# Performance work log

Hardware: AMD Instinct MI355X
Metric: run time of the kernel (lower is better)

Reference implementation:

```python
import jax, jax.numpy as jnp
import numpy as np

VOCAB = 32000
DIM = 1024
HID = 4096
MAXLEN = 2048
NH = 2       # number of sequential LowRankLinearAttention layers
KD = 64      # key_dim hardcoded in the module
B = 2
L = 2048


def setup_inputs() -> dict:
    key = jax.random.key(0)
    ks = jax.random.split(key, 12)
    def rn(k, shape, scale):
        return jax.random.normal(k, shape, dtype=jnp.float32) * scale
    return {
        "input_indices": jax.random.randint(ks[0], (B, L), 0, VOCAB),
        "token_embed": rn(ks[1], (VOCAB, DIM), 0.02),
        "pos_embed": rn(ks[2], (MAXLEN, DIM), 0.02),
        # per-layer attention projections (stored [in, out]; x @ W == torch Linear)
        "Wq": rn(ks[3], (NH, DIM, KD), DIM ** -0.5),
        "Wk": rn(ks[4], (NH, DIM, KD), DIM ** -0.5),
        "Wv": rn(ks[5], (NH, DIM, KD), DIM ** -0.5),
        "Wo": rn(ks[6], (NH, KD, DIM), KD ** -0.5),
        "norm_g": jnp.ones((NH, DIM), jnp.float32),
        "norm_b": jnp.zeros((NH, DIM), jnp.float32),
        "out_norm_g": jnp.ones((DIM,), jnp.float32),
        "out_norm_b": jnp.zeros((DIM,), jnp.float32),
        "W1": rn(ks[7], (DIM, HID), DIM ** -0.5),
        "b1": jnp.zeros((HID,), jnp.float32),
        "W2": rn(ks[8], (HID, VOCAB), HID ** -0.5),
        "b2": jnp.zeros((VOCAB,), jnp.float32),
    }


def _layernorm(x, g, b, eps=1e-5):
    m = jnp.mean(x, axis=-1, keepdims=True)
    v = jnp.var(x, axis=-1, keepdims=True)
    return (x - m) / jnp.sqrt(v + eps) * g + b


def _lowrank_linear_attn(x, Wq, Wk, Wv, Wo):
    # x: [B,L,D]; Q,K,V: [B,L,k]
    Q = jax.nn.elu(x @ Wq) + 1.0
    K = jax.nn.elu(x @ Wk) + 1.0
    V = x @ Wv
    # causal prefix sums of outer products K_t V_t^T -> [B,L,k,k]
    KV_sum = jnp.cumsum(K[..., :, None] * V[..., None, :], axis=1)
    K_sum = jnp.cumsum(K, axis=1)
    num = jnp.einsum('blk,blkj->blj', Q, KV_sum)          # [B,L,k]
    den = jnp.einsum('blk,blk->bl', Q, K_sum)[..., None]  # [B,L,1]
    return (num / (den + 1e-6)) @ Wo


def reference(input_indices, token_embed, pos_embed, Wq, Wk, Wv, Wo,
              norm_g, norm_b, out_norm_g, out_norm_b, W1, b1, W2, b2):
    seq_len = input_indices.shape[1]
    x = token_embed[input_indices] + pos_embed[jnp.arange(seq_len)]
    for i in range(Wq.shape[0]):
        x = x + _lowrank_linear_attn(x, Wq[i], Wk[i], Wv[i], Wo[i])
        x = _layernorm(x, norm_g[i], norm_b[i])
    x = _layernorm(x, out_norm_g, out_norm_b)
    h = jax.nn.gelu(x @ W1 + b1, approximate=False)  # torch nn.GELU default = erf
    logits = h @ W2 + b2
    return logits
```

## Files before the change

### kernel.cpp

```cpp
#include <hip/hip_runtime.h>

typedef __attribute__((ext_vector_type(4))) float  f4;
typedef __attribute__((ext_vector_type(2))) float  f2;
typedef __attribute__((ext_vector_type(4))) unsigned short us4;
typedef __attribute__((ext_vector_type(8))) short  s8;
typedef __attribute__((ext_vector_type(4))) float  f32x4;

__device__ __forceinline__ unsigned short f2bf(float f) {
  unsigned u = __float_as_uint(f);
  u += 0x7fffu + ((u >> 16) & 1u);
  return (unsigned short)(u >> 16);
}
__device__ __forceinline__ float elu1(float x) { return x > 0.f ? x + 1.f : __expf(x); }
__device__ __forceinline__ float gelu_erf(float x) { return 0.5f * x * (1.f + erff(x * 0.70710678118654752f)); }

__device__ __forceinline__ void async16(const void* g, void* l) {
  __builtin_amdgcn_global_load_lds((const __attribute__((address_space(1))) void*)g,
                                   (__attribute__((address_space(3))) void*)l, 16, 0, 0);
}

__device__ __forceinline__ unsigned l2u(const void* p) {
  return (unsigned)(size_t)(const __attribute__((address_space(3))) char*)p;
}
template<int OFF>
__device__ __forceinline__ void dsr(s8& d, unsigned base) {
  asm volatile("ds_read_b128 %0, %1 offset:%2" : "=v"(d) : "v"(base), "i"(OFF));
}
template<int KB>
__device__ __forceinline__ void readA8(s8 (&af)[8], unsigned base) {
  dsr<(0 * 2 + KB) * 1024>(af[0], base);
  dsr<(1 * 2 + KB) * 1024>(af[1], base);
  dsr<(2 * 2 + KB) * 1024>(af[2], base);
  dsr<(3 * 2 + KB) * 1024>(af[3], base);
  dsr<(4 * 2 + KB) * 1024>(af[4], base);
  dsr<(5 * 2 + KB) * 1024>(af[5], base);
  dsr<(6 * 2 + KB) * 1024>(af[6], base);
  dsr<(7 * 2 + KB) * 1024>(af[7], base);
}

__global__ __launch_bounds__(256) void embed_kernel(
    const int* __restrict__ idx, const float* __restrict__ tok,
    const float* __restrict__ pos, float* __restrict__ X, unsigned short* __restrict__ XB)
{
  int g = blockIdx.x * 256 + threadIdx.x;
  int t = g >> 8;
  int c4 = (g & 255) * 4;
  int l = t & 2047;
  int tk = idx[t];
  f4 v = *(const f4*)(tok + (size_t)tk * 1024 + c4);
  f4 p = *(const f4*)(pos + (size_t)l * 1024 + c4);
  v += p;
  *(f4*)(X + (size_t)t * 1024 + c4) = v;
  us4 o = { f2bf(v[0]), f2bf(v[1]), f2bf(v[2]), f2bf(v[3]) };
  *(us4*)(XB + (size_t)t * 1024 + c4) = o;
}

__global__ __launch_bounds__(256) void transpose_cvt(
    const float* __restrict__ src, unsigned short* __restrict__ dst, int N, int K)
{
  __shared__ unsigned short t[64][72];
  int k0 = blockIdx.x * 64, n0 = blockIdx.y * 64;
  int tid = threadIdx.x;
#pragma unroll
  for (int i = 0; i < 4; ++i) {
    int f = tid + i * 256;
    int r = f >> 4, c4 = (f & 15) * 4;
    f4 v = *(const f4*)(src + (size_t)(k0 + r) * N + n0 + c4);
    us4 o = { f2bf(v[0]), f2bf(v[1]), f2bf(v[2]), f2bf(v[3]) };
    *(us4*)&t[r][c4] = o;
  }
  __syncthreads();
#pragma unroll
  for (int i = 0; i < 4; ++i) {
    int f = tid + i * 256;
    int nr = f >> 4, kc4 = (f & 15) * 4;
    us4 o = { t[kc4 + 0][nr], t[kc4 + 1][nr], t[kc4 + 2][nr], t[kc4 + 3][nr] };
    *(us4*)(dst + (size_t)(n0 + nr) * K + k0 + kc4) = o;
  }
}

template<int EPI, int BF32>
__global__ __launch_bounds__(256) void gemm_bt(
    const unsigned short* __restrict__ A, const unsigned short* __restrict__ Bt,
    const float* __restrict__ Bf, const float* __restrict__ bias,
    void* __restrict__ Cv, int M, int N, int K, int mtiles)
{
  __shared__ unsigned short As[128 * 32];
  __shared__ unsigned short Bs[128 * 32];
  int bid = blockIdx.x;
  int mt = bid % mtiles, nt = bid / mtiles;
  int m0 = mt * 128, n0 = nt * 128;
  int tid = threadIdx.x, lane = tid & 63, w = tid >> 6;
  int wm = (w & 1) * 64, wn = (w >> 1) * 64;

  int c0 = w * 128 + lane, c1 = c0 + 64;
  size_t aO0 = (size_t)(m0 + (c0 >> 2)) * K + (size_t)((c0 & 3) * 8);
  size_t aO1 = (size_t)(m0 + (c1 >> 2)) * K + (size_t)((c1 & 3) * 8);
  size_t bO0 = (size_t)(n0 + (c0 >> 2)) * K + (size_t)((c0 & 3) * 8);
  size_t bO1 = (size_t)(n0 + (c1 >> 2)) * K + (size_t)((c1 & 3) * 8);
  unsigned short* lA0 = As + (w * 128) * 8;
  unsigned short* lA1 = As + (w * 128 + 64) * 8;
  unsigned short* lB0 = Bs + (w * 128) * 8;
  unsigned short* lB1 = Bs + (w * 128 + 64) * 8;

  f32x4 acc[4][4];
  f32x4 zz = {0.f, 0.f, 0.f, 0.f};
#pragma unroll
  for (int i = 0; i < 4; ++i)
#pragma unroll
    for (int j = 0; j < 4; ++j) acc[i][j] = zz;

  int rr = lane & 15, kh = (lane >> 4) * 8;
  const unsigned short* Ar = As + (wm + rr) * 32 + kh;
  const unsigned short* Br = Bs + (wn + rr) * 32 + kh;

  for (int k0 = 0; k0 < K; k0 += 32) {
    async16(A + aO0 + k0, lA0);
    async16(A + aO1 + k0, lA1);
    if constexpr (!BF32) {
      async16(Bt + bO0 + k0, lB0);
      async16(Bt + bO1 + k0, lB1);
    } else {
#pragma unroll
      for (int i = 0; i < 4; ++i) {
        int f = tid + i * 256;
        int kr = f >> 5, c4 = (f & 31) * 4;
        f4 v = *(const f4*)(Bf + (size_t)(k0 + kr) * N + n0 + c4);
#pragma unroll
        for (int e = 0; e < 4; ++e) Bs[(c4 + e) * 32 + kr] = f2bf(v[e]);
      }
    }
    __syncthreads();
    s8 af[4], bfr[4];
#pragma unroll
    for (int mi = 0; mi < 4; ++mi) af[mi] = *(const s8*)(Ar + mi * 512);
#pragma unroll
    for (int ni = 0; ni < 4; ++ni) bfr[ni] = *(const s8*)(Br + ni * 512);
#pragma unroll
    for (int mi = 0; mi < 4; ++mi)
#pragma unroll
      for (int ni = 0; ni < 4; ++ni)
        acc[mi][ni] = __builtin_amdgcn_mfma_f32_16x16x32_bf16(af[mi], bfr[ni], acc[mi][ni], 0, 0, 0);
    __syncthreads();
  }

  int cr = (lane >> 4) * 4;
#pragma unroll
  for (int mi = 0; mi < 4; ++mi) {
#pragma unroll
    for (int ni = 0; ni < 4; ++ni) {
      int gc = n0 + wn + ni * 16 + rr;
      float bv = (EPI > 0) ? bias[gc] : 0.f;
#pragma unroll
      for (int r = 0; r < 4; ++r) {
        int gr = m0 + wm + mi * 16 + cr + r;
        float v = acc[mi][ni][r] + bv;
        if constexpr (EPI == 1) {
          ((unsigned short*)Cv)[(size_t)gr * N + gc] = f2bf(gelu_erf(v));
        } else {
          ((float*)Cv)[(size_t)gr * N + gc] = v;
        }
      }
    }
  }
}

template<int RA, int RDKB, int RDNH, int ACCN, typename STG>
__device__ __forceinline__ void phaseX(
    unsigned ArdB, unsigned BrdB,
    s8 (&afDst)[8], s8 (&bfDst)[2],
    const s8 (&afUse)[8], const s8 (&bfUse)[2],
    f32x4 (&acc)[8][4], STG stg)
{
  dsr<((RDNH * 2 + 0) * 2 + RDKB) * 1024>(bfDst[0], BrdB);
  dsr<((RDNH * 2 + 1) * 2 + RDKB) * 1024>(bfDst[1], BrdB);
  if constexpr (RA) readA8<RDKB>(afDst, ArdB);
  stg();
  asm volatile("s_waitcnt vmcnt(6)" ::: "memory");
  __builtin_amdgcn_s_barrier();
  if constexpr (RA) asm volatile("s_waitcnt lgkmcnt(10)" ::: "memory");
  else              asm volatile("s_waitcnt lgkmcnt(2)" ::: "memory");
  __builtin_amdgcn_sched_barrier(0);
  __builtin_amdgcn_s_setprio(1);
#pragma unroll
  for (int f = 0; f < 8; ++f) {
    acc[f][ACCN * 2 + 0] =
        __builtin_amdgcn_mfma_f32_16x16x32_bf16(afUse[f], bfUse[0], acc[f][ACCN * 2 + 0], 0, 0, 0);
    acc[f][ACCN * 2 + 1] =
        __builtin_amdgcn_mfma_f32_16x16x32_bf16(afUse[f], bfUse[1], acc[f][ACCN * 2 + 1], 0, 0, 0);
  }
  __builtin_amdgcn_s_setprio(0);
  __builtin_amdgcn_sched_barrier(0);
}

template<int EPI>
__global__ __launch_bounds__(512, 2) void gemm256(
    const unsigned short* __restrict__ A, const unsigned short* __restrict__ Bt,
    const float* __restrict__ bias, void* __restrict__ Cv,
    int M, int N, int K, int mtiles)
{
  __shared__ __align__(16) char A0r[32768];
  __shared__ __align__(16) char B0r[32768];
  __shared__ __align__(16) char A1r[32768];
  __shared__ __align__(16) char B1r[32768];

  const int tid = threadIdx.x, lane = tid & 63, w = tid >> 6;
  const int wm = w >> 2, wn = w & 3;
  const int NT = K >> 6;

  int nwg = gridDim.x, orig = blockIdx.x;
  int q = nwg >> 3, r = nwg & 7;
  int xcd = orig & 7, lin = orig >> 3;
  int swz = (xcd < r ? xcd * (q + 1) : r * (q + 1) + (xcd - r) * q) + lin;
  int mt = swz % mtiles, nt = swz / mtiles;
  int m0 = mt * 256, n0 = nt * 256;

  const size_t klane8 = (size_t)((lane >> 4) << 3);
  const size_t arow0 = (size_t)(m0 + w * 32 + (lane & 15)) * K;
  const size_t arow1 = arow0 + (size_t)16 * K;
  const size_t brow0 = (size_t)(n0 + w * 32 + (lane & 15)) * K;
  const size_t brow1 = brow0 + (size_t)16 * K;
  const int stgoff = w * 4096;

  auto stgA = [&](char* reg, int kt, int kb) {
    int ktc = kt < NT ? kt : NT - 1;
    size_t kk = (size_t)ktc * 64 + (size_t)(kb * 32) + klane8;
    char* d = reg + stgoff + kb * 1024;
    async16(A + arow0 + kk, d);
    async16(A + arow1 + kk, d + 2048);
  };
  auto stgB = [&](char* reg, int kt, int kb) {
    int ktc = kt < NT ? kt : NT - 1;
    size_t kk = (size_t)ktc * 64 + (size_t)(kb * 32) + klane8;
    char* d = reg + stgoff + kb * 1024;
    async16(Bt + brow0 + kk, d);
    async16(Bt + brow1 + kk, d + 2048);
  };

  const unsigned AB0 = l2u(A0r + wm * 16384 + lane * 16);
  const unsigned BB0 = l2u(B0r + wn * 8192 + lane * 16);
  const unsigned AB1 = l2u(A1r + wm * 16384 + lane * 16);
  const unsigned BB1 = l2u(B1r + wn * 8192 + lane * 16);

  f32x4 acc[8][4];
  f32x4 zz = {0.f, 0.f, 0.f, 0.f};
#pragma unroll
  for (int i = 0; i < 8; ++i)
#pragma unroll
    for (int j = 0; j < 4; ++j) acc[i][j] = zz;
  s8 afA[8], afB[8], bfA[2], bfB[2];

  stgA(A0r, 0, 0); stgB(B0r, 0, 0);
  stgA(A0r, 0, 1); stgB(B0r, 0, 1);
  stgA(A1r, 1, 0); stgB(B1r, 1, 0);
  asm volatile("s_waitcnt vmcnt(8)" ::: "memory");
  __builtin_amdgcn_s_barrier();
  readA8<0>(afA, AB0);
  dsr<0>(bfA[0], BB0);
  dsr<2048>(bfA[1], BB0);

  for (int te = 0; te < NT; te += 2) {
    phaseX<0, 0, 1, 0>(AB0, BB0, afA, bfB, afA, bfA, acc, [&] { stgA(A1r, te + 1, 1); });
    phaseX<1, 1, 1, 1>(AB0, BB0, afB, bfA, afA, bfB, acc, [&] { stgB(B1r, te + 1, 1); });
    phaseX<0, 1, 0, 1>(AB0, BB0, afA, bfB, afB, bfA, acc, [&] { stgA(A0r, te + 2, 0); });
    phaseX<1, 0, 0, 0>(AB1, BB1, afA, bfA, afB, bfB, acc, [&] { stgB(B0r, te + 2, 0); });
    phaseX<0, 0, 1, 0>(AB1, BB1, afA, bfB, afA, bfA, acc, [&] { stgA(A0r, te + 2, 1); });
    phaseX<1, 1, 1, 1>(AB1, BB1, afB, bfA, afA, bfB, acc, [&] { stgB(B0r, te + 2, 1); });
    phaseX<0, 1, 0, 1>(AB1, BB1, afA, bfB, afB, bfA, acc, [&] { stgA(A1r, te + 3, 0); });
    phaseX<1, 0, 0, 0>(AB0, BB0, afA, bfA, afB, bfB, acc, [&] { stgB(B1r, te + 3, 0); });
  }

  asm volatile("s_waitcnt vmcnt(0) lgkmcnt(0)" ::: "memory");
  __builtin_amdgcn_sched_barrier(0);

  int rr = lane & 15, cr = (lane >> 4) * 4;
#pragma unroll
  for (int f = 0; f < 8; ++f) {
#pragma unroll
    for (int ni = 0; ni < 4; ++ni) {
      int gc = n0 + wn * 64 + ni * 16 + rr;
      float bv = bias[gc];
#pragma unroll
      for (int rg = 0; rg < 4; ++rg) {
        int gr = m0 + wm * 128 + f * 16 + cr + rg;
        float v = acc[f][ni][rg] + bv;
        if constexpr (EPI == 1) {
          ((unsigned short*)Cv)[(size_t)gr * N + gc] = f2bf(gelu_erf(v));
        } else {
          ((float*)Cv)[(size_t)gr * N + gc] = v;
        }
      }
    }
  }
}

__global__ __launch_bounds__(256) void chunk_sums(
    const float* __restrict__ QKV, float* __restrict__ KVc, float* __restrict__ Ksum)
{
  __shared__ float Ks[64][68], Vs[64][68];
  int blk = blockIdx.x, t0 = blk * 64, tid = threadIdx.x;
#pragma unroll
  for (int i = 0; i < 4; ++i) {
    int f = tid + i * 256;
    int r = f >> 4, c4 = (f & 15) * 4;
    const float* s = QKV + (size_t)(t0 + r) * 256;
    f4 k = *(const f4*)(s + 64 + c4);
    f4 v = *(const f4*)(s + 128 + c4);
#pragma unroll
    for (int e = 0; e < 4; ++e) { Ks[r][c4 + e] = elu1(k[e]); Vs[r][c4 + e] = v[e]; }
  }
  __syncthreads();
  int i0 = tid >> 2, jb = (tid & 3) * 16;
  f4 a0 = {0,0,0,0}, a1 = {0,0,0,0}, a2 = {0,0,0,0}, a3 = {0,0,0,0};
  for (int t = 0; t < 64; ++t) {
    float kk = Ks[t][i0];
    a0 += kk * (*(const f4*)&Vs[t][jb]);
    a1 += kk * (*(const f4*)&Vs[t][jb + 4]);
    a2 += kk * (*(const f4*)&Vs[t][jb + 8]);
    a3 += kk * (*(const f4*)&Vs[t][jb + 12]);
  }
  float* d = KVc + (size_t)blk * 4096 + i0 * 64 + jb;
  *(f4*)(d) = a0; *(f4*)(d + 4) = a1; *(f4*)(d + 8) = a2; *(f4*)(d + 12) = a3;
  if (tid < 64) {
    float s = 0.f;
    for (int t = 0; t < 64; ++t) s += Ks[t][tid];
    Ksum[(size_t)blk * 64 + tid] = s;
  }
}

__global__ __launch_bounds__(256) void prefix_state(
    const float* __restrict__ KVc, const float* __restrict__ Ksum,
    float* __restrict__ KVp, float* __restrict__ Ksump)
{
  int b = blockIdx.x >> 3, seg = blockIdx.x & 7;
  int e = seg * 512 + threadIdx.x * 2;
  f2 run = {0.f, 0.f};
#pragma unroll
  for (int c = 0; c < 32; ++c) {
    size_t base = ((size_t)b * 32 + c) * 4096 + e;
    *(f2*)(KVp + base) = run;
    run += *(const f2*)(KVc + base);
  }
  if (seg == 0 && threadIdx.x < 64) {
    float rs = 0.f; int i = threadIdx.x;
#pragma unroll
    for (int c = 0; c < 32; ++c) {
      size_t base = ((size_t)b * 32 + c) * 64 + i;
      Ksump[base] = rs;
      rs += Ksum[base];
    }
  }
}

__global__ __launch_bounds__(256) void attn_ns(
    const float* __restrict__ QKV, const float* __restrict__ KVp,
    const float* __restrict__ Ksump, float* __restrict__ NsG)
{
  __shared__ float Qs[64][68], Ks[64][68], Vs[64][68], Ss[64][68], Ps[64][68];
  __shared__ float ksps[64];
  int blk = blockIdx.x, t0 = blk * 64, tid = threadIdx.x;
#pragma unroll
  for (int i = 0; i < 4; ++i) {
    int f = tid + i * 256;
    int r = f >> 4, c4 = (f & 15) * 4;
    const float* s = QKV + (size_t)(t0 + r) * 256;
    f4 q = *(const f4*)(s + c4);
    f4 k = *(const f4*)(s + 64 + c4);
    f4 v = *(const f4*)(s + 128 + c4);
    f4 p = *(const f4*)(KVp + (size_t)blk * 4096 + r * 64 + c4);
#pragma unroll
    for (int e = 0; e < 4; ++e) {
      Qs[r][c4 + e] = elu1(q[e]); Ks[r][c4 + e] = elu1(k[e]);
      Vs[r][c4 + e] = v[e];       Ps[r][c4 + e] = p[e];
    }
  }
  if (tid < 64) ksps[tid] = Ksump[(size_t)blk * 64 + tid];
  __syncthreads();
  int tq = tid >> 2, jb = (tid & 3) * 16;
#pragma unroll
  for (int jj = 0; jj < 16; ++jj) {
    int tk = jb + jj;
    float s = 0.f;
    if (tk <= tq) {
#pragma unroll
      for (int k4 = 0; k4 < 16; ++k4) {
        f4 q = *(const f4*)&Qs[tq][k4 * 4];
        f4 k = *(const f4*)&Ks[tk][k4 * 4];
        s += q[0] * k[0] + q[1] * k[1] + q[2] * k[2] + q[3] * k[3];
      }
    }
    Ss[tq][tk] = s;
  }
  __syncthreads();
  f4 a0 = {0,0,0,0}, a1 = {0,0,0,0}, a2 = {0,0,0,0}, a3 = {0,0,0,0};
  for (int t = 0; t < 64; ++t) {
    float s = Ss[tq][t];
    a0 += s * (*(const f4*)&Vs[t][jb]);
    a1 += s * (*(const f4*)&Vs[t][jb + 4]);
    a2 += s * (*(const f4*)&Vs[t][jb + 8]);
    a3 += s * (*(const f4*)&Vs[t][jb + 12]);
  }
  for (int k = 0; k < 64; ++k) {
    float q = Qs[tq][k];
    a0 += q * (*(const f4*)&Ps[k][jb]);
    a1 += q * (*(const f4*)&Ps[k][jb + 4]);
    a2 += q * (*(const f4*)&Ps[k][jb + 8]);
    a3 += q * (*(const f4*)&Ps[k][jb + 12]);
  }
  float den = 0.f;
  for (int t = 0; t < 64; ++t) den += Ss[tq][t];
  for (int k = 0; k < 64; ++k) den += Qs[tq][k] * ksps[k];
  float inv = 1.f / (den + 1e-6f);
  float* d = NsG + (size_t)(t0 + tq) * 64 + jb;
  *(f4*)(d)      = a0 * inv;
  *(f4*)(d + 4)  = a1 * inv;
  *(f4*)(d + 8)  = a2 * inv;
  *(f4*)(d + 12) = a3 * inv;
}

__global__ __launch_bounds__(256) void attn_apply(
    const float* __restrict__ NsG, const float* __restrict__ Wo, float* __restrict__ X)
{
  __shared__ float Ns[64][68];
  __shared__ float Wt[64][260];
  int chunk = blockIdx.x >> 2, dg = blockIdx.x & 3;
  int t0 = chunk * 64, d0 = dg * 256, tid = threadIdx.x;
#pragma unroll
  for (int i = 0; i < 4; ++i) {
    int f = tid + i * 256;
    int r = f >> 4, c4 = (f & 15) * 4;
    *(f4*)&Ns[r][c4] = *(const f4*)(NsG + (size_t)(t0 + r) * 64 + c4);
  }
#pragma unroll
  for (int i = 0; i < 16; ++i) {
    int f = tid + i * 256;
    int r = f >> 6, c4 = (f & 63) * 4;
    *(f4*)&Wt[r][c4] = *(const f4*)(Wo + (size_t)r * 1024 + d0 + c4);
  }
  __syncthreads();
  int w = tid >> 6, lane = tid & 63;
  for (int ts = 0; ts < 16; ++ts) {
    int t = w * 16 + ts;
    float a0 = 0.f, a1 = 0.f, a2 = 0.f, a3 = 0.f;
#pragma unroll
    for (int j = 0; j < 64; ++j) {
      float nv = Ns[t][j];
      a0 += nv * Wt[j][lane];
      a1 += nv * Wt[j][64 + lane];
      a2 += nv * Wt[j][128 + lane];
      a3 += nv * Wt[j][192 + lane];
    }
    size_t o = (size_t)(t0 + t) * 1024 + d0 + lane;
    X[o]       += a0;
    X[o + 64]  += a1;
    X[o + 128] += a2;
    X[o + 192] += a3;
  }
}

__global__ __launch_bounds__(256) void layernorm_kernel(
    float* __restrict__ X, unsigned short* __restrict__ XB,
    const float* __restrict__ g, const float* __restrict__ b)
{
  int t = blockIdx.x * 4 + (threadIdx.x >> 6);
  int lane = threadIdx.x & 63;
  float* row = X + (size_t)t * 1024;
  f4 v[4];
  float s = 0.f, s2 = 0.f;
#pragma unroll
  for (int i = 0; i < 4; ++i) {
    v[i] = *(const f4*)(row + (i * 64 + lane) * 4);
#pragma unroll
    for (int e = 0; e < 4; ++e) { s += v[i][e]; s2 += v[i][e] * v[i][e]; }
  }
#pragma unroll
  for (int off = 32; off > 0; off >>= 1) {
    s  += __shfl_xor(s, off, 64);
    s2 += __shfl_xor(s2, off, 64);
  }
  float mean = s * (1.f / 1024.f);
  float var = s2 * (1.f / 1024.f) - mean * mean;
  float rstd = rsqrtf(var + 1e-5f);
#pragma unroll
  for (int i = 0; i < 4; ++i) {
    int d = (i * 64 + lane) * 4;
    f4 gv = *(const f4*)(g + d);
    f4 bv = *(const f4*)(b + d);
    f4 y;
#pragma unroll
    for (int e = 0; e < 4; ++e) y[e] = (v[i][e] - mean) * rstd * gv[e] + bv[e];
    *(f4*)(row + d) = y;
    us4 o = { f2bf(y[0]), f2bf(y[1]), f2bf(y[2]), f2bf(y[3]) };
    *(us4*)(XB + (size_t)t * 1024 + d) = o;
  }
}

extern "C" void kernel_launch(void* const* d_in, const int* in_sizes, int n_in,
                              void* d_out, int out_size, void* d_ws, size_t ws_size,
                              hipStream_t stream) {
  (void)in_sizes; (void)n_in; (void)out_size;
  const int*   idx = (const int*)d_in[0];
  const float* tok = (const float*)d_in[1];
  const float* pos = (const float*)d_in[2];
  const float* Wq  = (const float*)d_in[3];
  const float* Wk  = (const float*)d_in[4];
  const float* Wv  = (const float*)d_in[5];
  const float* Wo  = (const float*)d_in[6];
  const float* ng  = (const float*)d_in[7];
  const float* nb  = (const float*)d_in[8];
  const float* ong = (const float*)d_in[9];
  const float* onb = (const float*)d_in[10];
  const float* W1  = (const float*)d_in[11];
  const float* b1  = (const float*)d_in[12];
  const float* W2  = (const float*)d_in[13];
  const float* b2  = (const float*)d_in[14];
  float* out = (float*)d_out;
  char* ws = (char*)d_ws;

  float* X            = (float*)(ws + 0);
  unsigned short* XB  = (unsigned short*)(ws + 16777216);
  unsigned short* QT0 = (unsigned short*)(ws + 25165824);
  unsigned short* QT1 = (unsigned short*)(ws + 25690112);
  float* QKVB         = (float*)(ws + 26214400);
  float* KVC          = (float*)(ws + 30408704);
  float* KSUM         = (float*)(ws + 31457280);
  float* KVP          = (float*)(ws + 31490048);
  float* KSP          = (float*)(ws + 32538624);
  unsigned short* W1T = (unsigned short*)(ws + 32571392);
  unsigned short* H   = (unsigned short*)(ws + 40960000);
  unsigned short* W2T = (unsigned short*)(ws + 74514432);
  float* NSG = KVC;
  bool bigws = ws_size >= 336658432ull;

  hipMemsetAsync(QT0, 0, 524288, stream);
  hipMemsetAsync(QT1, 0, 524288, stream);
  transpose_cvt<<<dim3(16, 1), 256, 0, stream>>>(Wq,          QT0,              64, 1024);
  transpose_cvt<<<dim3(16, 1), 256, 0, stream>>>(Wk,          QT0 + 64 * 1024,  64, 1024);
  transpose_cvt<<<dim3(16, 1), 256, 0, stream>>>(Wv,          QT0 + 128 * 1024, 64, 1024);
  transpose_cvt<<<dim3(16, 1), 256, 0, stream>>>(Wq + 65536,  QT1,              64, 1024);
  transpose_cvt<<<dim3(16, 1), 256, 0, stream>>>(Wk + 65536,  QT1 + 64 * 1024,  64, 1024);
  transpose_cvt<<<dim3(16, 1), 256, 0, stream>>>(Wv + 65536,  QT1 + 128 * 1024, 64, 1024);
  transpose_cvt<<<dim3(16, 64), 256, 0, stream>>>(W1, W1T, 4096, 1024);
  if (bigws)
    transpose_cvt<<<dim3(64, 500), 256, 0, stream>>>(W2, W2T, 32000, 4096);

  embed_kernel<<<4096, 256, 0, stream>>>(idx, tok, pos, X, XB);

  for (int layer = 0; layer < 2; ++layer) {
    const unsigned short* QT = layer ? QT1 : QT0;
    gemm_bt<0, 0><<<64, 256, 0, stream>>>(XB, QT, nullptr, nullptr, QKVB, 4096, 256, 1024, 32);
    chunk_sums<<<64, 256, 0, stream>>>(QKVB, KVC, KSUM);
    prefix_state<<<16, 256, 0, stream>>>(KVC, KSUM, KVP, KSP);
    attn_ns<<<64, 256, 0, stream>>>(QKVB, KVP, KSP, NSG);
    attn_apply<<<256, 256, 0, stream>>>(NSG, Wo + (size_t)layer * 65536, X);
    layernorm_kernel<<<1024, 256, 0, stream>>>(X, XB, ng + layer * 1024, nb + layer * 1024);
  }
  layernorm_kernel<<<1024, 256, 0, stream>>>(X, XB, ong, onb);

  gemm256<1><<<256, 512, 0, stream>>>(XB, W1T, b1, H, 4096, 4096, 1024, 16);
  if (bigws)
    gemm256<2><<<2000, 512, 0, stream>>>(H, W2T, b2, out, 4096, 32000, 4096, 16);
  else
    gemm_bt<2, 1><<<8000, 256, 0, stream>>>(H, nullptr, W2, b2, out, 4096, 32000, 4096, 32);
}
```

Measured before the change: 1.653 ms.

## Switch big GEMM to 32x32x16 MFMA with per-k-slice LDS layout

Rewrites the 256x256 GEMM inner loop to use 32x32x16 bf16 MFMA instructions instead of 16x16x32, changing the LDS staging layout and fragment reads to match. The register double-buffering of A/B fragments across phases is dropped: each phase now reads its fragments, waits for all LDS reads, computes, and adds a second barrier. The aim is fewer MFMA issues and LDS reads per FLOP, at the cost of less overlap between LDS reads and MFMA plus extra barriers per phase.

```diff
diff --git a/kernel.cpp b/kernel.cpp
--- a/kernel.cpp
+++ b/kernel.cpp
@@ -5,6 +5,7 @@
 typedef __attribute__((ext_vector_type(4))) unsigned short us4;
 typedef __attribute__((ext_vector_type(8))) short  s8;
 typedef __attribute__((ext_vector_type(4))) float  f32x4;
+typedef __attribute__((ext_vector_type(16))) float f32x16;
 
 __device__ __forceinline__ unsigned short f2bf(float f) {
   unsigned u = __float_as_uint(f);
@@ -26,17 +27,8 @@
 __device__ __forceinline__ void dsr(s8& d, unsigned base) {
   asm volatile("ds_read_b128 %0, %1 offset:%2" : "=v"(d) : "v"(base), "i"(OFF));
 }
-template<int KB>
-__device__ __forceinline__ void readA8(s8 (&af)[8], unsigned base) {
-  dsr<(0 * 2 + KB) * 1024>(af[0], base);
-  dsr<(1 * 2 + KB) * 1024>(af[1], base);
-  dsr<(2 * 2 + KB) * 1024>(af[2], base);
-  dsr<(3 * 2 + KB) * 1024>(af[3], base);
-  dsr<(4 * 2 + KB) * 1024>(af[4], base);
-  dsr<(5 * 2 + KB) * 1024>(af[5], base);
-  dsr<(6 * 2 + KB) * 1024>(af[6], base);
-  dsr<(7 * 2 + KB) * 1024>(af[7], base);
-}
+
+#define MFMA32(a, b, c) __builtin_amdgcn_mfma_f32_32x32x16_bf16(a, b, c, 0, 0, 0)
 
 __global__ __launch_bounds__(256) void embed_kernel(
     const int* __restrict__ idx, const float* __restrict__ tok,
@@ -165,32 +157,33 @@
   }
 }
 
-template<int RA, int RDKB, int RDNH, int ACCN, typename STG>
-__device__ __forceinline__ void phaseX(
-    unsigned ArdB, unsigned BrdB,
-    s8 (&afDst)[8], s8 (&bfDst)[2],
-    const s8 (&afUse)[8], const s8 (&bfUse)[2],
-    f32x4 (&acc)[8][4], STG stg)
-{
-  dsr<((RDNH * 2 + 0) * 2 + RDKB) * 1024>(bfDst[0], BrdB);
-  dsr<((RDNH * 2 + 1) * 2 + RDKB) * 1024>(bfDst[1], BrdB);
-  if constexpr (RA) readA8<RDKB>(afDst, ArdB);
+template<int KS, int WAITV, typename STG>
+__device__ __forceinline__ void phase32(
+    unsigned AB, unsigned BB, f32x16 (&acc)[4][2], STG stg)
+{
+  s8 a0, a1, a2, a3, b0, b1;
+  dsr<(0 * 4 + KS) * 1024>(a0, AB);
+  dsr<(1 * 4 + KS) * 1024>(a1, AB);
+  dsr<(2 * 4 + KS) * 1024>(a2, AB);
+  dsr<(3 * 4 + KS) * 1024>(a3, AB);
+  dsr<(0 * 4 + KS) * 1024>(b0, BB);
+  dsr<(1 * 4 + KS) * 1024>(b1, BB);
   stg();
-  asm volatile("s_waitcnt vmcnt(6)" ::: "memory");
   __builtin_amdgcn_s_barrier();
-  if constexpr (RA) asm volatile("s_waitcnt lgkmcnt(10)" ::: "memory");
-  else              asm volatile("s_waitcnt lgkmcnt(2)" ::: "memory");
+  asm volatile("s_waitcnt lgkmcnt(0)" ::: "memory");
   __builtin_amdgcn_sched_barrier(0);
   __builtin_amdgcn_s_setprio(1);
-#pragma unroll
-  for (int f = 0; f < 8; ++f) {
-    acc[f][ACCN * 2 + 0] =
-        __builtin_amdgcn_mfma_f32_16x16x32_bf16(afUse[f], bfUse[0], acc[f][ACCN * 2 + 0], 0, 0, 0);
-    acc[f][ACCN * 2 + 1] =
-        __builtin_amdgcn_mfma_f32_16x16x32_bf16(afUse[f], bfUse[1], acc[f][ACCN * 2 + 1], 0, 0, 0);
-  }
+  acc[0][0] = MFMA32(a0, b0, acc[0][0]);
+  acc[1][0] = MFMA32(a1, b0, acc[1][0]);
+  acc[2][0] = MFMA32(a2, b0, acc[2][0]);
+  acc[3][0] = MFMA32(a3, b0, acc[3][0]);
+  acc[0][1] = MFMA32(a0, b1, acc[0][1]);
+  acc[1][1] = MFMA32(a1, b1, acc[1][1]);
+  acc[2][1] = MFMA32(a2, b1, acc[2][1]);
+  acc[3][1] = MFMA32(a3, b1, acc[3][1]);
   __builtin_amdgcn_s_setprio(0);
-  __builtin_amdgcn_sched_barrier(0);
+  if constexpr (WAITV) asm volatile("s_waitcnt vmcnt(8)" ::: "memory");
+  __builtin_amdgcn_s_barrier();
 }
 
 template<int EPI>
@@ -215,26 +208,23 @@
   int mt = swz % mtiles, nt = swz / mtiles;
   int m0 = mt * 256, n0 = nt * 256;
 
-  const size_t klane8 = (size_t)((lane >> 4) << 3);
-  const size_t arow0 = (size_t)(m0 + w * 32 + (lane & 15)) * K;
-  const size_t arow1 = arow0 + (size_t)16 * K;
-  const size_t brow0 = (size_t)(n0 + w * 32 + (lane & 15)) * K;
-  const size_t brow1 = brow0 + (size_t)16 * K;
-  const int stgoff = w * 4096;
-
-  auto stgA = [&](char* reg, int kt, int kb) {
+  const size_t klA = (size_t)((lane >> 5) << 3);
+  const size_t arowW = (size_t)(m0 + w * 32 + (lane & 31)) * K;
+  const size_t browW = (size_t)(n0 + w * 32 + (lane & 31)) * K;
+
+  auto stgA = [&](char* reg, int kt, int ksh) {
     int ktc = kt < NT ? kt : NT - 1;
-    size_t kk = (size_t)ktc * 64 + (size_t)(kb * 32) + klane8;
-    char* d = reg + stgoff + kb * 1024;
-    async16(A + arow0 + kk, d);
-    async16(A + arow1 + kk, d + 2048);
+    size_t c = (size_t)ktc * 64 + (size_t)(ksh * 32) + klA;
+    char* d = reg + (w * 4 + ksh * 2) * 1024;
+    async16(A + arowW + c, d);
+    async16(A + arowW + c + 16, d + 1024);
   };
-  auto stgB = [&](char* reg, int kt, int kb) {
+  auto stgB = [&](char* reg, int kt, int ksh) {
     int ktc = kt < NT ? kt : NT - 1;
-    size_t kk = (size_t)ktc * 64 + (size_t)(kb * 32) + klane8;
-    char* d = reg + stgoff + kb * 1024;
-    async16(Bt + brow0 + kk, d);
-    async16(Bt + brow1 + kk, d + 2048);
+    size_t c = (size_t)ktc * 64 + (size_t)(ksh * 32) + klA;
+    char* d = reg + (w * 4 + ksh * 2) * 1024;
+    async16(Bt + browW + c, d);
+    async16(Bt + browW + c + 16, d + 1024);
   };
 
   const unsigned AB0 = l2u(A0r + wm * 16384 + lane * 16);
@@ -242,48 +232,45 @@
   const unsigned AB1 = l2u(A1r + wm * 16384 + lane * 16);
   const unsigned BB1 = l2u(B1r + wn * 8192 + lane * 16);
 
-  f32x4 acc[8][4];
-  f32x4 zz = {0.f, 0.f, 0.f, 0.f};
-#pragma unroll
-  for (int i = 0; i < 8; ++i)
-#pragma unroll
-    for (int j = 0; j < 4; ++j) acc[i][j] = zz;
-  s8 afA[8], afB[8], bfA[2], bfB[2];
+  f32x16 acc[4][2];
+#pragma unroll
+  for (int i = 0; i < 4; ++i)
+#pragma unroll
+    for (int j = 0; j < 2; ++j)
+#pragma unroll
+      for (int e = 0; e < 16; ++e) acc[i][j][e] = 0.f;
 
   stgA(A0r, 0, 0); stgB(B0r, 0, 0);
   stgA(A0r, 0, 1); stgB(B0r, 0, 1);
   stgA(A1r, 1, 0); stgB(B1r, 1, 0);
   asm volatile("s_waitcnt vmcnt(8)" ::: "memory");
   __builtin_amdgcn_s_barrier();
-  readA8<0>(afA, AB0);
-  dsr<0>(bfA[0], BB0);
-  dsr<2048>(bfA[1], BB0);
 
   for (int te = 0; te < NT; te += 2) {
-    phaseX<0, 0, 1, 0>(AB0, BB0, afA, bfB, afA, bfA, acc, [&] { stgA(A1r, te + 1, 1); });
-    phaseX<1, 1, 1, 1>(AB0, BB0, afB, bfA, afA, bfB, acc, [&] { stgB(B1r, te + 1, 1); });
-    phaseX<0, 1, 0, 1>(AB0, BB0, afA, bfB, afB, bfA, acc, [&] { stgA(A0r, te + 2, 0); });
-    phaseX<1, 0, 0, 0>(AB1, BB1, afA, bfA, afB, bfB, acc, [&] { stgB(B0r, te + 2, 0); });
-    phaseX<0, 0, 1, 0>(AB1, BB1, afA, bfB, afA, bfA, acc, [&] { stgA(A0r, te + 2, 1); });
-    phaseX<1, 1, 1, 1>(AB1, BB1, afB, bfA, afA, bfB, acc, [&] { stgB(B0r, te + 2, 1); });
-    phaseX<0, 1, 0, 1>(AB1, BB1, afA, bfB, afB, bfA, acc, [&] { stgA(A1r, te + 3, 0); });
-    phaseX<1, 0, 0, 0>(AB0, BB0, afA, bfA, afB, bfB, acc, [&] { stgB(B1r, te + 3, 0); });
+    phase32<0, 0>(AB0, BB0, acc, [&] { stgA(A1r, te + 1, 1); });
+    phase32<1, 1>(AB0, BB0, acc, [&] { stgB(B1r, te + 1, 1); });
+    phase32<2, 0>(AB0, BB0, acc, [&] { stgA(A0r, te + 2, 0); });
+    phase32<3, 1>(AB0, BB0, acc, [&] { stgB(B0r, te + 2, 0); });
+    phase32<0, 0>(AB1, BB1, acc, [&] { stgA(A0r, te + 2, 1); });
+    phase32<1, 1>(AB1, BB1, acc, [&] { stgB(B0r, te + 2, 1); });
+    phase32<2, 0>(AB1, BB1, acc, [&] { stgA(A1r, te + 3, 0); });
+    phase32<3, 1>(AB1, BB1, acc, [&] { stgB(B1r, te + 3, 0); });
   }
 
   asm volatile("s_waitcnt vmcnt(0) lgkmcnt(0)" ::: "memory");
   __builtin_amdgcn_sched_barrier(0);
 
-  int rr = lane & 15, cr = (lane >> 4) * 4;
-#pragma unroll
-  for (int f = 0; f < 8; ++f) {
-#pragma unroll
-    for (int ni = 0; ni < 4; ++ni) {
-      int gc = n0 + wn * 64 + ni * 16 + rr;
+  int cl = lane & 31, rb = (lane >> 5) * 4;
+#pragma unroll
+  for (int mi = 0; mi < 4; ++mi) {
+#pragma unroll
+    for (int ni = 0; ni < 2; ++ni) {
+      int gc = n0 + wn * 64 + ni * 32 + cl;
       float bv = bias[gc];
 #pragma unroll
-      for (int rg = 0; rg < 4; ++rg) {
-        int gr = m0 + wm * 128 + f * 16 + cr + rg;
-        float v = acc[f][ni][rg] + bv;
+      for (int rg = 0; rg < 16; ++rg) {
+        int gr = m0 + wm * 128 + mi * 32 + (rg & 3) + 8 * (rg >> 2) + rb;
+        float v = acc[mi][ni][rg] + bv;
         if constexpr (EPI == 1) {
           ((unsigned short*)Cv)[(size_t)gr * N + gc] = f2bf(gelu_erf(v));
         } else {
```

After: 1.779 ms. 1.08x slower.
